# Kernel optimization log

Measured on AMD Instinct MI355X. Metric: run time of the kernel, lower is better.

## Reference

```python
import jax, jax.numpy as jnp
import numpy as np

B, N, D, C = 256, 200000, 128, 1000


def _l2_normalize(v, axis=-1, eps=1e-12):
    # matches torch F.normalize(p=2): v / max(||v||, eps)
    norm = jnp.sqrt(jnp.sum(v * v, axis=axis, keepdims=True))
    return v / jnp.maximum(norm, eps)


def setup_inputs() -> dict:
    key = jax.random.key(0)
    k1, k2, k3 = jax.random.split(key, 3)
    x = jax.random.normal(k1, (B, D), dtype=jnp.float32)
    index_embeddings = jax.random.normal(k2, (N, D), dtype=jnp.float32)
    class_labels = jax.random.randint(k3, (N,), 0, C, dtype=jnp.int32)
    return {
        "x": x,
        "index_embeddings": index_embeddings,
        "class_labels": class_labels,
        "num_classes": C,
    }


def reference(x, index_embeddings, class_labels, num_classes):
    # backbone output flattened -> embeddings [B, D]; L2-normalize (queries and index,
    # index normalization happens in add_index_data in the original module)
    emb = _l2_normalize(x)
    idx_emb = _l2_normalize(index_embeddings)
    # cosine similarities [B, N]
    similarities = jnp.einsum('bd,nd->bn', emb, idx_emb)
    # per-class max reduction (replaces Python loop over classes):
    # segment-max over the index dimension keyed by class_labels -> [B, num_classes]
    logits = jax.ops.segment_max(
        similarities.T, class_labels, num_segments=num_classes,
        indices_are_sorted=False,
    ).T
    return logits
```

## Files before the change

kernel.cpp:

```cpp
#include <hip/hip_runtime.h>
#include <hip/hip_bf16.h>
#include <stdint.h>

#define D_ 128
#define NB 64

typedef float f32x4 __attribute__((ext_vector_type(4)));
typedef short bf16x8 __attribute__((ext_vector_type(8)));

__device__ inline unsigned short f2bf(float f){
  unsigned x = __float_as_uint(f);
  return (unsigned short)((x + 0x7FFFu + ((x >> 16) & 1u)) >> 16);
}
__device__ inline unsigned packbf(float a, float b){
  return (unsigned)f2bf(a) | ((unsigned)f2bf(b) << 16);
}
__device__ inline unsigned fkey(float v){
  unsigned b = __float_as_uint(v);
  return (b & 0x80000000u) ? ~b : (b | 0x80000000u);
}

__global__ void k_norm_x(const float* __restrict__ x, unsigned short* __restrict__ xn){
  int row = blockIdx.x, lane = threadIdx.x;
  float2 v = reinterpret_cast<const float2*>(x + (size_t)row * D_)[lane];
  float ss = v.x * v.x + v.y * v.y;
  #pragma unroll
  for (int m = 1; m < 64; m <<= 1) ss += __shfl_xor(ss, m);
  float s = 1.0f / fmaxf(sqrtf(ss), 1e-12f);
  reinterpret_cast<unsigned*>(xn + (size_t)row * D_)[lane] = packbf(v.x * s, v.y * s);
}

__global__ void k_hist(const int* __restrict__ lab, unsigned* __restrict__ hist, int N, int C){
  __shared__ unsigned lh[1024];
  int t = threadIdx.x;
  for (int c = t; c < 1024; c += 256) lh[c] = 0;
  __syncthreads();
  for (int i = blockIdx.x * 256 + t; i < N; i += gridDim.x * 256)
    atomicAdd(&lh[lab[i]], 1u);
  __syncthreads();
  for (int c = t; c < C; c += 256) { unsigned v = lh[c]; if (v) atomicAdd(&hist[c], v); }
}

__global__ void k_scan(const unsigned* __restrict__ hist, unsigned* __restrict__ cursor, int C){
  __shared__ unsigned s[1024];
  int t = threadIdx.x;
  unsigned v = (t < C) ? hist[t] : 0u;
  s[t] = v; __syncthreads();
  for (int off = 1; off < 1024; off <<= 1){
    unsigned u = (t >= off) ? s[t - off] : 0u;
    __syncthreads();
    s[t] += u;
    __syncthreads();
  }
  if (t < C) cursor[t] = s[t] - v;
}

__global__ void k_scatter(const int* __restrict__ lab, unsigned* __restrict__ cursor,
                          int* __restrict__ perm, int* __restrict__ slab, int N){
  for (int i = blockIdx.x * 256 + threadIdx.x; i < N; i += gridDim.x * 256){
    int c = lab[i];
    unsigned pos = atomicAdd(&cursor[c], 1u);
    perm[pos] = i;
    slab[pos] = c;
  }
}

__global__ void k_init_out(unsigned* __restrict__ o, int n){
  int i = blockIdx.x * 256 + threadIdx.x;
  if (i < n) o[i] = 0x007FFFFFu;
}

struct __align__(16) GSm {
  unsigned short A[NB * 136];
  float sims[16 * 257];
  float scale[NB];
  int rowid[NB];
  int clab[NB];
};

__global__ __launch_bounds__(256, 2) void k_gemm(
    const float* __restrict__ emb, const unsigned short* __restrict__ xn,
    const int* __restrict__ perm, const int* __restrict__ slab,
    unsigned* __restrict__ out_u, int N, int C){
  __shared__ GSm sm;
  const int t = threadIdx.x;
  const int base = blockIdx.x * NB;

  if (t < NB){
    int p = base + t; if (p > N - 1) p = N - 1;
    sm.rowid[t] = perm[p];
    sm.clab[t]  = slab[p];
  }
  __syncthreads();

  {
    int r = t >> 2, j = t & 3;
    const float4* src = reinterpret_cast<const float4*>(emb + (long)sm.rowid[r] * D_ + j * 32);
    float4 v[8];
    #pragma unroll
    for (int i = 0; i < 8; i++) v[i] = src[i];
    float ss = 0.f;
    #pragma unroll
    for (int i = 0; i < 8; i++) ss += v[i].x*v[i].x + v[i].y*v[i].y + v[i].z*v[i].z + v[i].w*v[i].w;
    ss += __shfl_xor(ss, 1); ss += __shfl_xor(ss, 2);
    sm.scale[r] = 1.0f / fmaxf(sqrtf(ss), 1e-12f);
    unsigned* dst = reinterpret_cast<unsigned*>(&sm.A[r * 136 + j * 32]);
    #pragma unroll
    for (int i = 0; i < 8; i++){
      dst[i * 2]     = packbf(v[i].x, v[i].y);
      dst[i * 2 + 1] = packbf(v[i].z, v[i].w);
    }
  }

  const int w = t >> 6, lane = t & 63;
  const int lr = lane & 15, lg = lane >> 4;

  bf16x8 bf[4][4];
  #pragma unroll
  for (int ni = 0; ni < 4; ni++)
    #pragma unroll
    for (int kk = 0; kk < 4; kk++)
      bf[ni][kk] = *reinterpret_cast<const bf16x8*>(
          xn + (size_t)(w * 64 + ni * 16 + lr) * D_ + kk * 32 + lg * 8);

  f32x4 acc[4][4];
  #pragma unroll
  for (int mi = 0; mi < 4; mi++)
    #pragma unroll
    for (int ni = 0; ni < 4; ni++)
      acc[mi][ni] = (f32x4){0.f, 0.f, 0.f, 0.f};

  __syncthreads();

  #pragma unroll
  for (int mi = 0; mi < 4; mi++)
    #pragma unroll
    for (int kk = 0; kk < 4; kk++){
      bf16x8 af = *reinterpret_cast<const bf16x8*>(&sm.A[(mi * 16 + lr) * 136 + kk * 32 + lg * 8]);
      #pragma unroll
      for (int ni = 0; ni < 4; ni++)
        acc[mi][ni] = __builtin_amdgcn_mfma_f32_16x16x32_bf16(af, bf[ni][kk], acc[mi][ni], 0, 0, 0);
    }

  int cur = -1; float rm = 0.f;
  for (int mi = 0; mi < 4; mi++){
    __syncthreads();
    #pragma unroll
    for (int ni = 0; ni < 4; ni++)
      #pragma unroll
      for (int rg = 0; rg < 4; rg++){
        int r16 = lg * 4 + rg;
        sm.sims[r16 * 257 + w * 64 + ni * 16 + lr] = acc[mi][ni][rg] * sm.scale[mi * 16 + r16];
      }
    __syncthreads();
    #pragma unroll
    for (int r16 = 0; r16 < 16; r16++){
      int c = sm.clab[mi * 16 + r16];
      float v = sm.sims[r16 * 257 + t];
      if (c != cur){
        if (cur >= 0) atomicMax(&out_u[(size_t)t * C + cur], fkey(rm));
        cur = c; rm = v;
      } else rm = fmaxf(rm, v);
    }
  }
  atomicMax(&out_u[(size_t)t * C + cur], fkey(rm));
}

__global__ void k_finalize(unsigned* __restrict__ o, int n){
  int i = blockIdx.x * 256 + threadIdx.x;
  if (i < n){
    unsigned k = o[i];
    o[i] = (k & 0x80000000u) ? (k & 0x7FFFFFFFu) : ~k;
  }
}

extern "C" void kernel_launch(void* const* d_in, const int* in_sizes, int n_in,
                              void* d_out, int out_size, void* d_ws, size_t ws_size,
                              hipStream_t stream){
  const float* x   = (const float*)d_in[0];
  const float* emb = (const float*)d_in[1];
  const int*   lab = (const int*)d_in[2];
  const int B = in_sizes[0] / D_;
  const int N = in_sizes[1] / D_;
  const int C = out_size / B;

  char* ws = (char*)d_ws;
  unsigned short* xn = (unsigned short*)ws;
  size_t off = ((size_t)B * D_ * 2 + 255) & ~(size_t)255;
  unsigned* hist   = (unsigned*)(ws + off); off += 4096;
  unsigned* cursor = (unsigned*)(ws + off); off += 4096;
  int* perm = (int*)(ws + off); off += ((size_t)N * 4 + 255) & ~(size_t)255;
  int* slab = (int*)(ws + off);

  k_norm_x<<<B, 64, 0, stream>>>(x, xn);
  hipMemsetAsync(hist, 0, 8192, stream);
  k_hist<<<208, 256, 0, stream>>>(lab, hist, N, C);
  k_scan<<<1, 1024, 0, stream>>>(hist, cursor, C);
  k_scatter<<<208, 256, 0, stream>>>(lab, cursor, perm, slab, N);
  k_init_out<<<(B * C + 255) / 256, 256, 0, stream>>>((unsigned*)d_out, B * C);
  k_gemm<<<(N + NB - 1) / NB, 256, 0, stream>>>(emb, xn, perm, slab, (unsigned*)d_out, N, C);
  k_finalize<<<(B * C + 255) / 256, 256, 0, stream>>>((unsigned*)d_out, B * C);
}
```

Baseline: 288.1 us.

## Pre-normalize and permute embeddings to bf16, then stream sorted chunks with async LDS loads

A new pass normalizes each index row, converts it to bf16 and scatters it into class-sorted order, so the GEMM kernel reads contiguous bf16 chunks instead of gathering fp32 rows. The GEMM kernel handles several chunks per block, double-buffers them into swizzled LDS with global_load_lds, and reduces per-class maxima in registers using ballot-found segment boundaries. It also keeps up to eight class slots in registers before issuing atomics. In exchange it adds an extra full write and read of a bf16 copy of the index, and it needs enough workspace, otherwise it falls back to the old gather kernel.

```diff
diff --git a/kernel.cpp b/kernel.cpp
--- a/kernel.cpp
+++ b/kernel.cpp
@@ -4,6 +4,8 @@
 
 #define D_ 128
 #define NB 64
+#define KCH 4
+#define NINF (-__builtin_inff())
 
 typedef float f32x4 __attribute__((ext_vector_type(4)));
 typedef short bf16x8 __attribute__((ext_vector_type(8)));
@@ -56,18 +58,166 @@
 }
 
 __global__ void k_scatter(const int* __restrict__ lab, unsigned* __restrict__ cursor,
-                          int* __restrict__ perm, int* __restrict__ slab, int N){
+                          int* __restrict__ perm, int* __restrict__ slab,
+                          int* __restrict__ dstpos, int N){
   for (int i = blockIdx.x * 256 + threadIdx.x; i < N; i += gridDim.x * 256){
     int c = lab[i];
     unsigned pos = atomicAdd(&cursor[c], 1u);
     perm[pos] = i;
     slab[pos] = c;
+    dstpos[i] = (int)pos;
   }
 }
 
 __global__ void k_init_out(unsigned* __restrict__ o, int n){
   int i = blockIdx.x * 256 + threadIdx.x;
   if (i < n) o[i] = 0x007FFFFFu;
+}
+
+__global__ void k_permnorm(const float* __restrict__ emb, const int* __restrict__ dstpos,
+                           unsigned short* __restrict__ nrm, int N){
+  int r = blockIdx.x * 64 + (threadIdx.x >> 2);
+  if (r >= N) return;
+  int j = threadIdx.x & 3;
+  const f32x4* src = reinterpret_cast<const f32x4*>(emb + (size_t)r * D_ + j * 32);
+  f32x4 v[8];
+  #pragma unroll
+  for (int i = 0; i < 8; i++) v[i] = src[i];
+  float ss = 0.f;
+  #pragma unroll
+  for (int i = 0; i < 8; i++) ss += v[i][0]*v[i][0] + v[i][1]*v[i][1] + v[i][2]*v[i][2] + v[i][3]*v[i][3];
+  ss += __shfl_xor(ss, 1); ss += __shfl_xor(ss, 2);
+  float sc = 1.0f / fmaxf(sqrtf(ss), 1e-12f);
+  int d = dstpos[r];
+  unsigned o[16];
+  #pragma unroll
+  for (int i = 0; i < 8; i++){
+    o[i*2]   = packbf(v[i][0]*sc, v[i][1]*sc);
+    o[i*2+1] = packbf(v[i][2]*sc, v[i][3]*sc);
+  }
+  uint4* dst = reinterpret_cast<uint4*>(nrm + (size_t)d * D_ + j * 32);
+  #pragma unroll
+  for (int i = 0; i < 4; i++) dst[i] = make_uint4(o[i*4], o[i*4+1], o[i*4+2], o[i*4+3]);
+}
+
+__global__ __launch_bounds__(256, 3) void k_gemm(
+    const unsigned short* __restrict__ nrm,
+    const unsigned short* __restrict__ xn,
+    const int* __restrict__ slab,
+    unsigned* __restrict__ out_u,
+    int nchunks, int N, int C){
+  __shared__ __align__(16) unsigned short Ab[2][NB * D_];
+  const int t = threadIdx.x;
+  const int w = t >> 6, lane = t & 63, lr = lane & 15, lg = lane >> 4;
+
+  const int cbeg = blockIdx.x * KCH;
+  if (cbeg >= nchunks) return;
+  int cend = cbeg + KCH; if (cend > nchunks) cend = nchunks;
+
+  bf16x8 bf[4][4];
+  #pragma unroll
+  for (int ni = 0; ni < 4; ni++)
+    #pragma unroll
+    for (int kk = 0; kk < 4; kk++)
+      bf[ni][kk] = *reinterpret_cast<const bf16x8*>(
+          xn + (size_t)(w * 64 + ni * 16 + lr) * D_ + kk * 32 + lg * 8);
+
+  const int c0 = slab[(size_t)cbeg * NB];
+  float rT0=NINF, rT1=NINF, rT2=NINF, rT3=NINF, rT4=NINF, rT5=NINF, rT6=NINF, rT7=NINF;
+
+  auto stageF = [&](int cn, int bb){
+    const char* sb = (const char*)(nrm + (size_t)cn * NB * D_);
+    char* lb = (char*)(&Ab[bb][0]);
+    #pragma unroll
+    for (int i = 0; i < 4; i++){
+      int L = t * 16 + i * 4096;
+      int row = L >> 8, s = (L >> 4) & 15;
+      int so = row * 256 + ((s ^ (row & 7)) << 4);
+      __builtin_amdgcn_global_load_lds(
+          (const __attribute__((address_space(1))) unsigned int*)(sb + so),
+          (__attribute__((address_space(3))) unsigned int*)(lb + L),
+          16, 0, 0);
+    }
+  };
+
+  stageF(cbeg, 0);
+
+  for (int c = cbeg; c < cend; ++c){
+    const int b = (c - cbeg) & 1;
+    const int rowbase = c * NB;
+    int rb = rowbase + lane;
+    int myc = slab[rb < N ? rb : (N - 1)];
+    int nx = __shfl_down(myc, 1);
+    unsigned long long bmask = __ballot(lane < 63 && myc != nx);
+    asm volatile("s_waitcnt vmcnt(0)" ::: "memory");
+    if (c + 1 < cend) stageF(c + 1, b ^ 1);
+    asm volatile("s_barrier" ::: "memory");
+
+    f32x4 acc[4][4];
+    #pragma unroll
+    for (int mi = 0; mi < 4; mi++)
+      #pragma unroll
+      for (int ni = 0; ni < 4; ni++)
+        acc[mi][ni] = (f32x4){0.f, 0.f, 0.f, 0.f};
+
+    #pragma unroll
+    for (int mi = 0; mi < 4; mi++){
+      const int row = mi * 16 + lr;
+      const char* rp = (const char*)(&Ab[b][0]) + row * 256;
+      #pragma unroll
+      for (int kk = 0; kk < 4; kk++){
+        bf16x8 af = *reinterpret_cast<const bf16x8*>(rp + (((kk * 4 + lg) ^ (row & 7)) << 4));
+        #pragma unroll
+        for (int ni = 0; ni < 4; ni++)
+          acc[mi][ni] = __builtin_amdgcn_mfma_f32_16x16x32_bf16(af, bf[ni][kk], acc[mi][ni], 0, 0, 0);
+      }
+    }
+
+    int a = 0;
+    unsigned long long mm = bmask;
+    for (;;){
+      int e = mm ? (__builtin_ctzll(mm) + 1) : 64;
+      int cls = __shfl(myc, a);
+      float m0=NINF, m1=NINF, m2=NINF, m3=NINF;
+      #pragma unroll
+      for (int mi = 0; mi < 4; mi++)
+        #pragma unroll
+        for (int rg = 0; rg < 4; rg++){
+          int row = mi * 16 + lg * 4 + rg;
+          bool in = (row >= a) && (row < e) && (rowbase + row < N);
+          m0 = in ? fmaxf(m0, acc[mi][0][rg]) : m0;
+          m1 = in ? fmaxf(m1, acc[mi][1][rg]) : m1;
+          m2 = in ? fmaxf(m2, acc[mi][2][rg]) : m2;
+          m3 = in ? fmaxf(m3, acc[mi][3][rg]) : m3;
+        }
+      m0 = fmaxf(m0, __shfl_xor(m0, 16)); m0 = fmaxf(m0, __shfl_xor(m0, 32));
+      m1 = fmaxf(m1, __shfl_xor(m1, 16)); m1 = fmaxf(m1, __shfl_xor(m1, 32));
+      m2 = fmaxf(m2, __shfl_xor(m2, 16)); m2 = fmaxf(m2, __shfl_xor(m2, 32));
+      m3 = fmaxf(m3, __shfl_xor(m3, 16)); m3 = fmaxf(m3, __shfl_xor(m3, 32));
+      float mv = (lg < 2) ? ((lg == 0) ? m0 : m1) : ((lg == 2) ? m2 : m3);
+      int slot = cls - c0;
+      switch (slot){
+        case 0: rT0 = fmaxf(rT0, mv); break;
+        case 1: rT1 = fmaxf(rT1, mv); break;
+        case 2: rT2 = fmaxf(rT2, mv); break;
+        case 3: rT3 = fmaxf(rT3, mv); break;
+        case 4: rT4 = fmaxf(rT4, mv); break;
+        case 5: rT5 = fmaxf(rT5, mv); break;
+        case 6: rT6 = fmaxf(rT6, mv); break;
+        case 7: rT7 = fmaxf(rT7, mv); break;
+        default: atomicMax(&out_u[(size_t)t * C + cls], fkey(mv)); break;
+      }
+      if (e >= 64) break;
+      a = e; mm &= mm - 1;
+    }
+    asm volatile("s_barrier" ::: "memory");
+  }
+
+  const size_t ob = (size_t)t * C;
+  #define FLUSH(S_, V_) { int cls = c0 + S_; if (cls < C && V_ != NINF) atomicMax(&out_u[ob + cls], fkey(V_)); }
+  FLUSH(0, rT0) FLUSH(1, rT1) FLUSH(2, rT2) FLUSH(3, rT3)
+  FLUSH(4, rT4) FLUSH(5, rT5) FLUSH(6, rT6) FLUSH(7, rT7)
+  #undef FLUSH
 }
 
 struct __align__(16) GSm {
@@ -78,21 +228,19 @@
   int clab[NB];
 };
 
-__global__ __launch_bounds__(256, 2) void k_gemm(
+__global__ __launch_bounds__(256, 2) void k_gemm_gather(
     const float* __restrict__ emb, const unsigned short* __restrict__ xn,
     const int* __restrict__ perm, const int* __restrict__ slab,
     unsigned* __restrict__ out_u, int N, int C){
   __shared__ GSm sm;
   const int t = threadIdx.x;
   const int base = blockIdx.x * NB;
-
   if (t < NB){
     int p = base + t; if (p > N - 1) p = N - 1;
     sm.rowid[t] = perm[p];
     sm.clab[t]  = slab[p];
   }
   __syncthreads();
-
   {
     int r = t >> 2, j = t & 3;
     const float4* src = reinterpret_cast<const float4*>(emb + (long)sm.rowid[r] * D_ + j * 32);
@@ -111,27 +259,22 @@
       dst[i * 2 + 1] = packbf(v[i].z, v[i].w);
     }
   }
-
   const int w = t >> 6, lane = t & 63;
   const int lr = lane & 15, lg = lane >> 4;
-
-  bf16x8 bf[4][4];
+  bf16x8 bfr[4][4];
   #pragma unroll
   for (int ni = 0; ni < 4; ni++)
     #pragma unroll
     for (int kk = 0; kk < 4; kk++)
-      bf[ni][kk] = *reinterpret_cast<const bf16x8*>(
+      bfr[ni][kk] = *reinterpret_cast<const bf16x8*>(
           xn + (size_t)(w * 64 + ni * 16 + lr) * D_ + kk * 32 + lg * 8);
-
   f32x4 acc[4][4];
   #pragma unroll
   for (int mi = 0; mi < 4; mi++)
     #pragma unroll
     for (int ni = 0; ni < 4; ni++)
       acc[mi][ni] = (f32x4){0.f, 0.f, 0.f, 0.f};
-
   __syncthreads();
-
   #pragma unroll
   for (int mi = 0; mi < 4; mi++)
     #pragma unroll
@@ -139,9 +282,8 @@
       bf16x8 af = *reinterpret_cast<const bf16x8*>(&sm.A[(mi * 16 + lr) * 136 + kk * 32 + lg * 8]);
       #pragma unroll
       for (int ni = 0; ni < 4; ni++)
-        acc[mi][ni] = __builtin_amdgcn_mfma_f32_16x16x32_bf16(af, bf[ni][kk], acc[mi][ni], 0, 0, 0);
-    }
-
+        acc[mi][ni] = __builtin_amdgcn_mfma_f32_16x16x32_bf16(af, bfr[ni][kk], acc[mi][ni], 0, 0, 0);
+    }
   int cur = -1; float rm = 0.f;
   for (int mi = 0; mi < 4; mi++){
     __syncthreads();
@@ -183,21 +325,32 @@
   const int B = in_sizes[0] / D_;
   const int N = in_sizes[1] / D_;
   const int C = out_size / B;
+  const int nchunks = (N + NB - 1) / NB;
 
   char* ws = (char*)d_ws;
-  unsigned short* xn = (unsigned short*)ws;
-  size_t off = ((size_t)B * D_ * 2 + 255) & ~(size_t)255;
+  size_t off = 0;
+  unsigned short* xn = (unsigned short*)(ws); off += ((size_t)B * D_ * 2 + 255) & ~(size_t)255;
   unsigned* hist   = (unsigned*)(ws + off); off += 4096;
   unsigned* cursor = (unsigned*)(ws + off); off += 4096;
-  int* perm = (int*)(ws + off); off += ((size_t)N * 4 + 255) & ~(size_t)255;
-  int* slab = (int*)(ws + off);
+  size_t narr = ((size_t)N * 4 + 255) & ~(size_t)255;
+  int* perm   = (int*)(ws + off); off += narr;
+  int* slab   = (int*)(ws + off); off += narr;
+  int* dstpos = (int*)(ws + off); off += narr;
+  unsigned short* nrm = (unsigned short*)(ws + off);
+  size_t need = off + (size_t)nchunks * NB * D_ * 2;
+  const bool fast = (ws_size >= need);
 
   k_norm_x<<<B, 64, 0, stream>>>(x, xn);
   hipMemsetAsync(hist, 0, 8192, stream);
   k_hist<<<208, 256, 0, stream>>>(lab, hist, N, C);
   k_scan<<<1, 1024, 0, stream>>>(hist, cursor, C);
-  k_scatter<<<208, 256, 0, stream>>>(lab, cursor, perm, slab, N);
+  k_scatter<<<208, 256, 0, stream>>>(lab, cursor, perm, slab, dstpos, N);
   k_init_out<<<(B * C + 255) / 256, 256, 0, stream>>>((unsigned*)d_out, B * C);
-  k_gemm<<<(N + NB - 1) / NB, 256, 0, stream>>>(emb, xn, perm, slab, (unsigned*)d_out, N, C);
+  if (fast){
+    k_permnorm<<<(N + 63) / 64, 256, 0, stream>>>(emb, dstpos, nrm, N);
+    k_gemm<<<(nchunks + KCH - 1) / KCH, 256, 0, stream>>>(nrm, xn, slab, (unsigned*)d_out, nchunks, N, C);
+  } else {
+    k_gemm_gather<<<nchunks, 256, 0, stream>>>(emb, xn, perm, slab, (unsigned*)d_out, N, C);
+  }
   k_finalize<<<(B * C + 255) / 256, 256, 0, stream>>>((unsigned*)d_out, B * C);
 }
```

Result: no change. 292.6 us (+1.6%).
